# Optimization experiments

Hardware: AMD Instinct MI355X
Metric: run time of the kernel (lower is better)

## Reference

```python
import jax, jax.numpy as jnp
import numpy as np

B, S, D, H = 2, 2048, 1024, 16
DH = D // H
ROPE_BASE = 10000.0


def apply_rope(x):
    # x: [B, H, S, DH]; rotate-half RoPE, base 10000
    half = DH // 2
    inv_freq = 1.0 / (ROPE_BASE ** (jnp.arange(half, dtype=jnp.float32) / half))
    ang = jnp.arange(S, dtype=jnp.float32)[:, None] * inv_freq[None, :]  # [S, half]
    cos = jnp.cos(ang)[None, None]  # [1,1,S,half]
    sin = jnp.sin(ang)[None, None]
    x1, x2 = x[..., :half], x[..., half:]
    return jnp.concatenate([x1 * cos - x2 * sin, x1 * sin + x2 * cos], axis=-1)


def setup_inputs() -> dict:
    key = jax.random.key(0)
    ks = jax.random.split(key, 9)
    w = lambda k: jax.random.normal(k, (D, D), dtype=jnp.float32) * 0.02
    return {
        "x": jax.random.normal(ks[0], (B, S, D), dtype=jnp.float32),
        "Wq": w(ks[1]), "bq": jnp.zeros((D,), jnp.float32),
        "Wk": w(ks[2]), "bk": jnp.zeros((D,), jnp.float32),
        "Wv": w(ks[3]), "bv": jnp.zeros((D,), jnp.float32),
        "Wo": w(ks[4]), "bo": jnp.zeros((D,), jnp.float32),
    }


def reference(x, Wq, bq, Wk, bk, Wv, bv, Wo, bo):
    # projections (W stored as [in, out])
    q = x @ Wq + bq
    k = x @ Wk + bk
    v = x @ Wv + bv
    # [B, S, D] -> [B, H, S, DH]
    to_heads = lambda t: t.reshape(B, S, H, DH).transpose(0, 2, 1, 3)
    q, k, v = to_heads(q), to_heads(k), to_heads(v)
    q = apply_rope(q)
    k = apply_rope(k)
    scores = jnp.einsum("bhqd,bhkd->bhqk", q, k) / jnp.sqrt(jnp.float32(DH))
    causal = jnp.tril(jnp.ones((S, S), dtype=bool))  # [S, S]
    scores = jnp.where(causal[None, None], scores, -jnp.inf)
    probs = jax.nn.softmax(scores, axis=-1)
    ctx = jnp.einsum("bhqk,bhkd->bhqd", probs, v)
    ctx = ctx.transpose(0, 2, 1, 3).reshape(B, S, D)  # concat heads
    return ctx @ Wo + bo
```

## Files before the change

### kernel.cpp

```cpp
#include <hip/hip_runtime.h>
#include <hip/hip_bf16.h>

#define B_  2
#define S_  2048
#define D_  1024
#define H_  16
#define DH_ 64

typedef __attribute__((ext_vector_type(8))) short bf16x8;
typedef __attribute__((ext_vector_type(4))) float f32x4;

__device__ __forceinline__ short f2bf(float f) {
  unsigned int u; __builtin_memcpy(&u, &f, 4);
  u = (u + 0x7FFFu + ((u >> 16) & 1u)) >> 16;
  return (short)u;
}
__device__ __forceinline__ unsigned cvtpk(float a, float b) {
  unsigned r;
  asm("v_cvt_pk_bf16_f32 %0, %1, %2" : "=v"(r) : "v"(a), "v"(b));
  return r;
}

#define GLOAD_LDS16(gp, lp) \
  __builtin_amdgcn_global_load_lds((const __attribute__((address_space(1))) void*)(gp), \
                                   (__attribute__((address_space(3))) void*)(lp), 16, 0, 0)

#define MFMA16(a, b, c) __builtin_amdgcn_mfma_f32_16x16x32_bf16(a, b, c, 0, 0, 0)

#define RAW_BARRIER() do {                                   \
    asm volatile("s_waitcnt lgkmcnt(0)" ::: "memory");       \
    __builtin_amdgcn_s_barrier();                            \
    asm volatile("" ::: "memory");                           \
  } while (0)

union U8 { unsigned u[4]; bf16x8 v; };

__global__ __launch_bounds__(256) void k_cvt_table(const float* __restrict__ in,
                                                   short* __restrict__ out,
                                                   float* __restrict__ cosT,
                                                   float* __restrict__ sinT) {
  int bid = blockIdx.x;
  if (bid < 4096) {
    int i = bid * 256 + threadIdx.x;
    float4 v = ((const float4*)in)[i];
    short4 o; o.x = f2bf(v.x); o.y = f2bf(v.y); o.z = f2bf(v.z); o.w = f2bf(v.w);
    *(short4*)(out + (size_t)i * 4) = o;
  } else {
    int i = (bid - 4096) * 256 + threadIdx.x;
    int s = i >> 5, d = i & 31;
    float invf = exp2f(-(float)d * (13.287712379549449f / 32.0f));
    float ang = (float)s * invf;
    cosT[i] = cosf(ang);
    sinT[i] = sinf(ang);
  }
}

__global__ __launch_bounds__(256) void k_transpose4(const float* __restrict__ W0,
                                                    const float* __restrict__ W1,
                                                    const float* __restrict__ W2,
                                                    const float* __restrict__ W3,
                                                    short* __restrict__ WtBase) {
  __shared__ float tile[32][33];
  const float* W = (blockIdx.z == 0) ? W0 : (blockIdx.z == 1) ? W1 :
                   (blockIdx.z == 2) ? W2 : W3;
  short* Wt = WtBase + (size_t)blockIdx.z * D_ * D_;
  int tx = threadIdx.x, ty = threadIdx.y;
  int bx = blockIdx.x * 32, by = blockIdx.y * 32;
  #pragma unroll
  for (int i = 0; i < 32; i += 8)
    tile[ty + i][tx] = W[(size_t)(by + ty + i) * D_ + bx + tx];
  __syncthreads();
  #pragma unroll
  for (int i = 0; i < 32; i += 8)
    Wt[(size_t)(bx + ty + i) * D_ + by + tx] = f2bf(tile[tx][ty + i]);
}

__global__ __launch_bounds__(256) void k_gemm_qkv(const short* __restrict__ A,
                                                  const short* __restrict__ Bt,
                                                  const float* __restrict__ bq,
                                                  const float* __restrict__ bk,
                                                  const float* __restrict__ bv,
                                                  const float* __restrict__ cosT,
                                                  const float* __restrict__ sinT,
                                                  short* __restrict__ qb,
                                                  short* __restrict__ kb,
                                                  short* __restrict__ vb) {
  const int K = 1024;
  __shared__ __align__(16) short lA[128 * 32];
  __shared__ __align__(16) short lB[128 * 32];
  const int fid = blockIdx.y * 24 + blockIdx.x;
  const int swz = (fid & 7) * 96 + (fid >> 3);
  const int bxs = swz % 24, bys = swz / 24;
  const int tid = threadIdx.x;
  const int wid = tid >> 6, lane = tid & 63;
  const int brow = bys * 128, bcol = bxs * 128;
  const int wr = wid >> 1, wc = wid & 1;
  const int g = lane >> 4, c15 = lane & 15;
  const int sr = lane >> 2, scol = (lane & 3) * 8;
  f32x4 acc[4][4] = {};

  for (int kt = 0; kt < K; kt += 32) {
    __syncthreads();
    #pragma unroll
    for (int ch = 0; ch < 2; ++ch) {
      const short* ga = A + (size_t)(brow + ch * 64 + wid * 16 + sr) * K + kt + scol;
      const short* gb = Bt + (size_t)(bcol + ch * 64 + wid * 16 + sr) * K + kt + scol;
      GLOAD_LDS16(ga, &lA[(ch * 64 + wid * 16) * 32]);
      GLOAD_LDS16(gb, &lB[(ch * 64 + wid * 16) * 32]);
    }
    __syncthreads();
    bf16x8 af[4], bfr[4];
    #pragma unroll
    for (int mi = 0; mi < 4; ++mi)
      af[mi] = *(const bf16x8*)&lA[(wr * 64 + mi * 16 + c15) * 32 + g * 8];
    #pragma unroll
    for (int ni = 0; ni < 4; ++ni)
      bfr[ni] = *(const bf16x8*)&lB[(wc * 64 + ni * 16 + c15) * 32 + g * 8];
    #pragma unroll
    for (int mi = 0; mi < 4; ++mi)
      #pragma unroll
      for (int ni = 0; ni < 4; ++ni)
        acc[mi][ni] = MFMA16(af[mi], bfr[ni], acc[mi][ni]);
  }

  const int seg = bcol >> 10;
  const float* bp = (seg == 0) ? bq : (seg == 1) ? bk : bv;
  short* dst = (seg == 0) ? qb : (seg == 1) ? kb : vb;
  const float alpha = (seg == 0) ? 0.18033688f : 1.0f;
  const bool rope = (seg < 2);
  #pragma unroll
  for (int mi = 0; mi < 4; ++mi) {
    #pragma unroll
    for (int ni = 0; ni < 2; ++ni) {
      int col  = bcol + wc * 64 + ni * 16 + c15;
      int lcol = col & 1023;
      int d    = col & 63;
      float b1 = bp[lcol], b2 = bp[lcol + 32];
      #pragma unroll
      for (int r = 0; r < 4; ++r) {
        int row = brow + wr * 64 + mi * 16 + g * 4 + r;
        float x1 = (acc[mi][ni][r]     + b1) * alpha;
        float x2 = (acc[mi][ni + 2][r] + b2) * alpha;
        float o1 = x1, o2 = x2;
        if (rope) {
          int s = row & (S_ - 1);
          float co = cosT[s * 32 + d], si = sinT[s * 32 + d];
          o1 = x1 * co - x2 * si;
          o2 = x1 * si + x2 * co;
        }
        dst[(size_t)row * 1024 + lcol]      = f2bf(o1);
        dst[(size_t)row * 1024 + lcol + 32] = f2bf(o2);
      }
    }
  }
}

__global__ __launch_bounds__(256) void k_gemm(const short* __restrict__ A,
                                              const short* __restrict__ Bt,
                                              const float* __restrict__ bias,
                                              float* __restrict__ out,
                                              int M, int N, int K) {
  __shared__ __align__(16) short lA[128 * 32];
  __shared__ __align__(16) short lB[128 * 32];
  const int fid = blockIdx.y * 8 + blockIdx.x;
  const int swz = (fid & 7) * 32 + (fid >> 3);
  const int bxs = swz % 8, bys = swz / 8;
  const int tid = threadIdx.x;
  const int wid = tid >> 6, lane = tid & 63;
  const int brow = bys * 128, bcol = bxs * 128;
  const int wr = wid >> 1, wc = wid & 1;
  const int g = lane >> 4, c15 = lane & 15;
  const int sr = lane >> 2, scol = (lane & 3) * 8;
  f32x4 acc[4][4] = {};

  for (int kt = 0; kt < K; kt += 32) {
    __syncthreads();
    #pragma unroll
    for (int ch = 0; ch < 2; ++ch) {
      const short* ga = A + (size_t)(brow + ch * 64 + wid * 16 + sr) * K + kt + scol;
      const short* gb = Bt + (size_t)(bcol + ch * 64 + wid * 16 + sr) * K + kt + scol;
      GLOAD_LDS16(ga, &lA[(ch * 64 + wid * 16) * 32]);
      GLOAD_LDS16(gb, &lB[(ch * 64 + wid * 16) * 32]);
    }
    __syncthreads();
    bf16x8 af[4], bfr[4];
    #pragma unroll
    for (int mi = 0; mi < 4; ++mi)
      af[mi] = *(const bf16x8*)&lA[(wr * 64 + mi * 16 + c15) * 32 + g * 8];
    #pragma unroll
    for (int ni = 0; ni < 4; ++ni)
      bfr[ni] = *(const bf16x8*)&lB[(wc * 64 + ni * 16 + c15) * 32 + g * 8];
    #pragma unroll
    for (int mi = 0; mi < 4; ++mi)
      #pragma unroll
      for (int ni = 0; ni < 4; ++ni)
        acc[mi][ni] = MFMA16(af[mi], bfr[ni], acc[mi][ni]);
  }

  #pragma unroll
  for (int mi = 0; mi < 4; ++mi) {
    #pragma unroll
    for (int ni = 0; ni < 4; ++ni) {
      int col = bcol + wc * 64 + ni * 16 + c15;
      float bv = bias[col];
      #pragma unroll
      for (int r = 0; r < 4; ++r) {
        int row = brow + wr * 64 + mi * 16 + g * 4 + r;
        out[(size_t)row * N + col] = acc[mi][ni][r] + bv;
      }
    }
  }
}

__device__ __forceinline__ void softmax_g(f32x4 (&s)[4], float& m, float& l,
                                          f32x4 (&o)[4], int g) {
  float pm = -1e30f;
  #pragma unroll
  for (int n = 0; n < 4; ++n)
    #pragma unroll
    for (int r = 0; r < 4; ++r) pm = fmaxf(pm, s[n][r]);
  pm = fmaxf(pm, __shfl_xor(pm, 16));
  pm = fmaxf(pm, __shfl_xor(pm, 32));
  if (!__all(pm <= m + 8.0f)) {
    float nm = fmaxf(m, pm);
    float corr = exp2f(m - nm);
    m = nm; l *= corr;
    float cf[4];
    #pragma unroll
    for (int r = 0; r < 4; ++r) cf[r] = __shfl(corr, g * 4 + r);
    #pragma unroll
    for (int dblk = 0; dblk < 4; ++dblk)
      #pragma unroll
      for (int r = 0; r < 4; ++r) o[dblk][r] *= cf[r];
  }
  float rs = 0.0f;
  #pragma unroll
  for (int n = 0; n < 4; ++n)
    #pragma unroll
    for (int r = 0; r < 4; ++r) {
      float p = exp2f(s[n][r] - m);
      s[n][r] = p; rs += p;
    }
  rs += __shfl_xor(rs, 16);
  rs += __shfl_xor(rs, 32);
  l += rs;
}

__device__ __forceinline__ void build_pa(const f32x4 (&s)[4], U8 (&pa)[2],
                                         int g, int c15) {
  unsigned pk[4][2];
  #pragma unroll
  for (int n = 0; n < 4; ++n) {
    pk[n][0] = cvtpk(s[n][0], s[n][1]);
    pk[n][1] = cvtpk(s[n][2], s[n][3]);
  }
  #pragma unroll
  for (int kh = 0; kh < 2; ++kh) {
    #pragma unroll
    for (int widx = 0; widx < 4; ++widx) {
      int src = (2 * (g & 1) + (widx >> 1)) * 16 + c15;
      unsigned lo = __shfl(pk[2 * kh][widx & 1], src);
      unsigned hi = __shfl(pk[2 * kh + 1][widx & 1], src);
      pa[kh].u[widx] = (g & 2) ? hi : lo;
    }
  }
}

__global__ __launch_bounds__(256, 4) void k_flash(const short* __restrict__ Qb,
                                                  const short* __restrict__ Kb,
                                                  const short* __restrict__ Vb,
                                                  short* __restrict__ Ctx,
                                                  float* __restrict__ pO,
                                                  float* __restrict__ pML) {
  __shared__ __align__(16) short Vt[2][64][72];
  __shared__ __align__(16) short Kl[2][4096];
  const int bid = blockIdx.x;
  const int sched = bid >> 5, bh = bid & 31;
  int qt, t0, t1, sid = 0; bool split;
  if (sched < 19) { qt = 18 - sched; t0 = 0; t1 = qt; split = false; }
  else {
    int j = sched - 19; qt = 31 - (j >> 1);
    int h1 = (qt + 2) >> 1;
    if ((j & 1) == 0) { t0 = h1; t1 = qt; }
    else              { t0 = 0;  t1 = h1 - 1; }
    split = true; sid = bh * 26 + j;
  }
  const int b   = bh >> 4, h = bh & 15;
  const int tid = threadIdx.x, w = tid >> 6, lane = tid & 63;
  const int g   = lane >> 4, c15 = lane & 15;
  const int qg0 = qt * 64 + w * 16;
  const int qabs = qg0 + c15;

  const short* qp = Qb + ((size_t)(b * S_ + qabs)) * D_ + h * DH_ + g * 8;
  bf16x8 qf0 = *(const bf16x8*)qp;
  bf16x8 qf1 = *(const bf16x8*)(qp + 32);

  const int vkv = lane;
  const int vd0 = w * 16;
  const int vcol = vkv ^ (w << 3);
  const short* vrow = Vb + (size_t)b * S_ * D_ + h * DH_ + vd0;

  const short* kbase = Kb + (size_t)b * S_ * D_ + h * DH_;
  const int kidx0 = w * 128 + lane;
  const int kkv0 = kidx0 >> 3, kdb0 = (kidx0 & 7) ^ (kkv0 & 7);
  const int kidx1 = kidx0 + 64;
  const int kkv1 = kidx1 >> 3, kdb1 = (kidx1 & 7) ^ (kkv1 & 7);

  f32x4 o[4] = {};
  float m = -1e30f, l = 0.0f;

  bf16x8 kc0, kc1, vc0, vc1, kn0, kn1, vn0, vn1;

  {
    const short* kb0 = kbase + (size_t)(t0 * 64) * D_;
    bf16x8 tk0 = *(const bf16x8*)(kb0 + (size_t)kkv0 * D_ + kdb0 * 8);
    bf16x8 tk1 = *(const bf16x8*)(kb0 + (size_t)kkv1 * D_ + kdb1 * 8);
    const short* vp = vrow + (size_t)(t0 * 64 + vkv) * D_;
    bf16x8 tv0 = *(const bf16x8*)vp;
    bf16x8 tv1 = *(const bf16x8*)(vp + 8);
    *(bf16x8*)&Kl[t0 & 1][kidx0 * 8] = tk0;
    *(bf16x8*)&Kl[t0 & 1][kidx1 * 8] = tk1;
    #pragma unroll
    for (int j = 0; j < 8; ++j) Vt[t0 & 1][vd0 + j][vcol] = tv0[j];
    #pragma unroll
    for (int j = 0; j < 8; ++j) Vt[t0 & 1][vd0 + 8 + j][vcol] = tv1[j];
    if (t0 + 1 <= t1) {
      const short* kb1 = kbase + (size_t)((t0 + 1) * 64) * D_;
      kc0 = *(const bf16x8*)(kb1 + (size_t)kkv0 * D_ + kdb0 * 8);
      kc1 = *(const bf16x8*)(kb1 + (size_t)kkv1 * D_ + kdb1 * 8);
      const short* vp1 = vrow + (size_t)((t0 + 1) * 64 + vkv) * D_;
      vc0 = *(const bf16x8*)vp1;
      vc1 = *(const bf16x8*)(vp1 + 8);
    }
  }
  RAW_BARRIER();

#define FBODY(T, KC0, KC1, VC0, VC1, KN0, KN1, VN0, VN1) do {                   \
    const int kv0 = (T) * 64;                                                   \
    if ((T) + 2 <= t1) {                                                        \
      const short* kb2 = kbase + (size_t)(kv0 + 128) * D_;                      \
      KN0 = *(const bf16x8*)(kb2 + (size_t)kkv0 * D_ + kdb0 * 8);               \
      KN1 = *(const bf16x8*)(kb2 + (size_t)kkv1 * D_ + kdb1 * 8);               \
      const short* vp2 = vrow + (size_t)(kv0 + 128 + vkv) * D_;                 \
      VN0 = *(const bf16x8*)vp2;                                                \
      VN1 = *(const bf16x8*)(vp2 + 8);                                          \
    }                                                                           \
    if (kv0 <= qg0 + 15) {                                                      \
      const short* ks = &Kl[(T) & 1][0];                                        \
      f32x4 s[4] = {};                                                          \
      __builtin_amdgcn_s_setprio(1);                                            \
      _Pragma("unroll")                                                         \
      for (int n = 0; n < 4; ++n) {                                             \
        int krow = (n * 16 + c15) * 64;                                         \
        bf16x8 k0 = *(const bf16x8*)&ks[krow + ((g ^ (c15 & 7)) * 8)];          \
        bf16x8 k1 = *(const bf16x8*)&ks[krow + (((g + 4) ^ (c15 & 7)) * 8)];    \
        s[n] = MFMA16(k0, qf0, s[n]);                                           \
        s[n] = MFMA16(k1, qf1, s[n]);                                           \
      }                                                                         \
      __builtin_amdgcn_s_setprio(0);                                            \
      if (kv0 + 63 > qg0) {                                                     \
        _Pragma("unroll")                                                       \
        for (int n = 0; n < 4; ++n)                                             \
          _Pragma("unroll")                                                     \
          for (int r = 0; r < 4; ++r)                                           \
            if (kv0 + n * 16 + g * 4 + r > qabs) s[n][r] = -1e30f;              \
      }                                                                         \
      softmax_g(s, m, l, o, g);                                                 \
      U8 pa[2];                                                                 \
      build_pa(s, pa, g, c15);                                                  \
      __builtin_amdgcn_s_setprio(1);                                            \
      _Pragma("unroll")                                                         \
      for (int kh = 0; kh < 2; ++kh)                                            \
        _Pragma("unroll")                                                       \
        for (int dblk = 0; dblk < 4; ++dblk) {                                  \
          bf16x8 vbf = *(const bf16x8*)&Vt[(T) & 1][dblk * 16 + c15]            \
                                         [kh * 32 + ((g ^ dblk) * 8)];          \
          o[dblk] = MFMA16(pa[kh].v, vbf, o[dblk]);                             \
        }                                                                       \
      __builtin_amdgcn_s_setprio(0);                                            \
    }                                                                           \
    if ((T) + 1 <= t1) {                                                        \
      *(bf16x8*)&Kl[((T) + 1) & 1][kidx0 * 8] = KC0;                            \
      *(bf16x8*)&Kl[((T) + 1) & 1][kidx1 * 8] = KC1;                            \
      _Pragma("unroll")                                                         \
      for (int j = 0; j < 8; ++j) Vt[((T) + 1) & 1][vd0 + j][vcol] = VC0[j];    \
      _Pragma("unroll")                                                         \
      for (int j = 0; j < 8; ++j) Vt[((T) + 1) & 1][vd0 + 8 + j][vcol] = VC1[j];\
      RAW_BARRIER();                                                            \
    }                                                                           \
  } while (0)

  for (int t = t0; t <= t1; ) {
    FBODY(t, kc0, kc1, vc0, vc1, kn0, kn1, vn0, vn1);
    ++t;
    if (t > t1) break;
    FBODY(t, kn0, kn1, vn0, vn1, kc0, kc1, vc0, vc1);
    ++t;
  }
#undef FBODY

  if (!split) {
    float linv = 1.0f / l;
    float lf[4];
    #pragma unroll
    for (int r = 0; r < 4; ++r) lf[r] = __shfl(linv, g * 4 + r);
    #pragma unroll
    for (int dblk = 0; dblk < 4; ++dblk)
      #pragma unroll
      for (int r = 0; r < 4; ++r) {
        int q = qg0 + g * 4 + r;
        Ctx[((size_t)(b * S_ + q)) * D_ + h * DH_ + dblk * 16 + c15] = f2bf(o[dblk][r] * lf[r]);
      }
  } else {
    float* po = pO + ((size_t)sid * 64 + w * 16) * 64;
    #pragma unroll
    for (int dblk = 0; dblk < 4; ++dblk)
      #pragma unroll
      for (int r = 0; r < 4; ++r)
        po[(g * 4 + r) * 64 + dblk * 16 + c15] = o[dblk][r];
    if (lane < 16) {
      pML[(size_t)sid * 128 + w * 16 + lane]      = m;
      pML[(size_t)sid * 128 + 64 + w * 16 + lane] = l;
    }
  }
}

__global__ __launch_bounds__(256) void k_combine(const float* __restrict__ pO,
                                                 const float* __restrict__ pML,
                                                 short* __restrict__ Ctx) {
  const int p = blockIdx.x;
  const int qt = 19 + (p >> 5), bh = p & 31;
  const int b = bh >> 4, h = bh & 15;
  const int jb = (31 - qt) * 2;
  const int sidB = bh * 26 + jb;
  const int sidA = bh * 26 + jb + 1;
  const int q = threadIdx.x >> 2;
  const int d0 = (threadIdx.x & 3) * 16;
  float mA = pML[(size_t)sidA * 128 + q], lA = pML[(size_t)sidA * 128 + 64 + q];
  float mB = pML[(size_t)sidB * 128 + q], lB = pML[(size_t)sidB * 128 + 64 + q];
  float M = fmaxf(mA, mB);
  float wA = exp2f(mA - M), wB = exp2f(mB - M);
  float inv = 1.0f / (lA * wA + lB * wB);
  const float* oA = pO + ((size_t)sidA * 64 + q) * 64 + d0;
  const float* oB = pO + ((size_t)sidB * 64 + q) * 64 + d0;
  short* cp = Ctx + ((size_t)(b * S_ + qt * 64 + q)) * D_ + h * DH_ + d0;
  #pragma unroll
  for (int i = 0; i < 16; i += 4) {
    float4 a = *(const float4*)(oA + i);
    float4 c = *(const float4*)(oB + i);
    cp[i + 0] = f2bf((a.x * wA + c.x * wB) * inv);
    cp[i + 1] = f2bf((a.y * wA + c.y * wB) * inv);
    cp[i + 2] = f2bf((a.z * wA + c.z * wB) * inv);
    cp[i + 3] = f2bf((a.w * wA + c.w * wB) * inv);
  }
}

extern "C" void kernel_launch(void* const* d_in, const int* in_sizes, int n_in,
                              void* d_out, int out_size, void* d_ws, size_t ws_size,
                              hipStream_t stream) {
  (void)in_sizes; (void)n_in; (void)out_size; (void)ws_size;
  const float* x  = (const float*)d_in[0];
  const float* Wq = (const float*)d_in[1];
  const float* bq = (const float*)d_in[2];
  const float* Wk = (const float*)d_in[3];
  const float* bk = (const float*)d_in[4];
  const float* Wv = (const float*)d_in[5];
  const float* bv = (const float*)d_in[6];
  const float* Wo = (const float*)d_in[7];
  const float* bo = (const float*)d_in[8];
  float* out = (float*)d_out;
  char* ws = (char*)d_ws;

  const size_t MS = (size_t)B_ * S_;
  short* xb  = (short*)(ws);
  short* wqT = (short*)(ws + (size_t)8 * 1024 * 1024);
  short* wkT = wqT + (size_t)D_ * D_;
  short* wvT = wkT + (size_t)D_ * D_;
  short* woT = wvT + (size_t)D_ * D_;
  short* qb  = (short*)(ws + (size_t)16 * 1024 * 1024);
  short* kb  = qb + MS * D_;
  short* vb  = kb + MS * D_;
  short* ctx = vb + MS * D_;
  float* cosT = (float*)(ws + (size_t)48 * 1024 * 1024);
  float* sinT = cosT + (size_t)S_ * 32;
  float* pO  = (float*)(ws);
  float* pML = (float*)(ws + (size_t)48 * 1024 * 1024 + 512 * 1024);

  k_cvt_table<<<dim3(4096 + 256), 256, 0, stream>>>(x, xb, cosT, sinT);
  k_transpose4<<<dim3(32, 32, 4), dim3(32, 8), 0, stream>>>(Wq, Wk, Wv, Wo, wqT);
  k_gemm_qkv<<<dim3(24, 32), 256, 0, stream>>>(xb, wqT, bq, bk, bv, cosT, sinT, qb, kb, vb);
  k_flash<<<dim3(45 * 32), 256, 0, stream>>>(qb, kb, vb, ctx, pO, pML);
  k_combine<<<dim3(13 * 32), 256, 0, stream>>>(pO, pML, ctx);
  k_gemm<<<dim3(8, 32), 256, 0, stream>>>(ctx, woT, bo, out, 4096, 1024, 1024);
}
```

Measured before the change: 135.6 us.

## Load K fragments directly from global memory instead of staging through LDS

Drops the double-buffered K shared-memory tile and its register prefetch. Each wave now reads its K MFMA operands straight from global memory (relying on L1/L2 to share them across the four waves), and the launch bound rises to 8 blocks per CU. The aim is to cut LDS footprint and register pressure so occupancy increases. The cost is that K loads are no longer prefetched, so their latency sits on the critical path before the QK MFMAs, each wave issues its own redundant global loads, and the per-wave causal skip of fully masked tiles is gone.

```diff
diff --git a/kernel.cpp b/kernel.cpp
--- a/kernel.cpp
+++ b/kernel.cpp
@@ -266,14 +266,13 @@
   }
 }
 
-__global__ __launch_bounds__(256, 4) void k_flash(const short* __restrict__ Qb,
+__global__ __launch_bounds__(256, 8) void k_flash(const short* __restrict__ Qb,
                                                   const short* __restrict__ Kb,
                                                   const short* __restrict__ Vb,
                                                   short* __restrict__ Ctx,
                                                   float* __restrict__ pO,
                                                   float* __restrict__ pML) {
   __shared__ __align__(16) short Vt[2][64][72];
-  __shared__ __align__(16) short Kl[2][4096];
   const int bid = blockIdx.x;
   const int sched = bid >> 5, bh = bid & 31;
   int qt, t0, t1, sid = 0; bool split;
@@ -295,39 +294,27 @@
   bf16x8 qf0 = *(const bf16x8*)qp;
   bf16x8 qf1 = *(const bf16x8*)(qp + 32);
 
+  const short* kbase = Kb + (size_t)b * S_ * D_ + h * DH_ + g * 8;
+
   const int vkv = lane;
   const int vd0 = w * 16;
   const int vcol = vkv ^ (w << 3);
   const short* vrow = Vb + (size_t)b * S_ * D_ + h * DH_ + vd0;
 
-  const short* kbase = Kb + (size_t)b * S_ * D_ + h * DH_;
-  const int kidx0 = w * 128 + lane;
-  const int kkv0 = kidx0 >> 3, kdb0 = (kidx0 & 7) ^ (kkv0 & 7);
-  const int kidx1 = kidx0 + 64;
-  const int kkv1 = kidx1 >> 3, kdb1 = (kidx1 & 7) ^ (kkv1 & 7);
-
   f32x4 o[4] = {};
   float m = -1e30f, l = 0.0f;
 
-  bf16x8 kc0, kc1, vc0, vc1, kn0, kn1, vn0, vn1;
+  bf16x8 vc0, vc1, vn0, vn1;
 
   {
-    const short* kb0 = kbase + (size_t)(t0 * 64) * D_;
-    bf16x8 tk0 = *(const bf16x8*)(kb0 + (size_t)kkv0 * D_ + kdb0 * 8);
-    bf16x8 tk1 = *(const bf16x8*)(kb0 + (size_t)kkv1 * D_ + kdb1 * 8);
     const short* vp = vrow + (size_t)(t0 * 64 + vkv) * D_;
     bf16x8 tv0 = *(const bf16x8*)vp;
     bf16x8 tv1 = *(const bf16x8*)(vp + 8);
-    *(bf16x8*)&Kl[t0 & 1][kidx0 * 8] = tk0;
-    *(bf16x8*)&Kl[t0 & 1][kidx1 * 8] = tk1;
     #pragma unroll
     for (int j = 0; j < 8; ++j) Vt[t0 & 1][vd0 + j][vcol] = tv0[j];
     #pragma unroll
     for (int j = 0; j < 8; ++j) Vt[t0 & 1][vd0 + 8 + j][vcol] = tv1[j];
     if (t0 + 1 <= t1) {
-      const short* kb1 = kbase + (size_t)((t0 + 1) * 64) * D_;
-      kc0 = *(const bf16x8*)(kb1 + (size_t)kkv0 * D_ + kdb0 * 8);
-      kc1 = *(const bf16x8*)(kb1 + (size_t)kkv1 * D_ + kdb1 * 8);
       const short* vp1 = vrow + (size_t)((t0 + 1) * 64 + vkv) * D_;
       vc0 = *(const bf16x8*)vp1;
       vc1 = *(const bf16x8*)(vp1 + 8);
@@ -335,25 +322,21 @@
   }
   RAW_BARRIER();
 
-#define FBODY(T, KC0, KC1, VC0, VC1, KN0, KN1, VN0, VN1) do {                   \
+#define FBODY(T, VC0, VC1, VN0, VN1) do {                                       \
     const int kv0 = (T) * 64;                                                   \
     if ((T) + 2 <= t1) {                                                        \
-      const short* kb2 = kbase + (size_t)(kv0 + 128) * D_;                      \
-      KN0 = *(const bf16x8*)(kb2 + (size_t)kkv0 * D_ + kdb0 * 8);               \
-      KN1 = *(const bf16x8*)(kb2 + (size_t)kkv1 * D_ + kdb1 * 8);               \
       const short* vp2 = vrow + (size_t)(kv0 + 128 + vkv) * D_;                 \
       VN0 = *(const bf16x8*)vp2;                                                \
       VN1 = *(const bf16x8*)(vp2 + 8);                                          \
     }                                                                           \
-    if (kv0 <= qg0 + 15) {                                                      \
-      const short* ks = &Kl[(T) & 1][0];                                        \
+    {                                                                           \
+      const short* kp = kbase + (size_t)(kv0 + c15) * D_;                       \
       f32x4 s[4] = {};                                                          \
       __builtin_amdgcn_s_setprio(1);                                            \
       _Pragma("unroll")                                                         \
       for (int n = 0; n < 4; ++n) {                                             \
-        int krow = (n * 16 + c15) * 64;                                         \
-        bf16x8 k0 = *(const bf16x8*)&ks[krow + ((g ^ (c15 & 7)) * 8)];          \
-        bf16x8 k1 = *(const bf16x8*)&ks[krow + (((g + 4) ^ (c15 & 7)) * 8)];    \
+        bf16x8 k0 = *(const bf16x8*)(kp + (size_t)n * 16 * D_);                 \
+        bf16x8 k1 = *(const bf16x8*)(kp + (size_t)n * 16 * D_ + 32);            \
         s[n] = MFMA16(k0, qf0, s[n]);                                           \
         s[n] = MFMA16(k1, qf1, s[n]);                                           \
       }                                                                         \
@@ -380,8 +363,6 @@
       __builtin_amdgcn_s_setprio(0);                                            \
     }                                                                           \
     if ((T) + 1 <= t1) {                                                        \
-      *(bf16x8*)&Kl[((T) + 1) & 1][kidx0 * 8] = KC0;                            \
-      *(bf16x8*)&Kl[((T) + 1) & 1][kidx1 * 8] = KC1;                            \
       _Pragma("unroll")                                                         \
       for (int j = 0; j < 8; ++j) Vt[((T) + 1) & 1][vd0 + j][vcol] = VC0[j];    \
       _Pragma("unroll")                                                         \
@@ -391,10 +372,10 @@
   } while (0)
 
   for (int t = t0; t <= t1; ) {
-    FBODY(t, kc0, kc1, vc0, vc1, kn0, kn1, vn0, vn1);
+    FBODY(t, vc0, vc1, vn0, vn1);
     ++t;
     if (t > t1) break;
-    FBODY(t, kn0, kn1, vn0, vn1, kc0, kc1, vc0, vc1);
+    FBODY(t, vn0, vn1, vc0, vc1);
     ++t;
   }
 #undef FBODY
```

Result: slower. 216.4 us (+59.6%).

## Double-buffer GEMM LDS tiles and merge prep kernels into one launch

Applied to the files above, without the earlier changes.

Both GEMM kernels now use two LDS buffers per operand. The next K-tile is issued via global_load_lds while the current tile is consumed by MFMAs, with a vmcnt wait and a single barrier per step in place of two syncthreads around a blocking load. Separately, the fp32-to-bf16 conversion/RoPE-table kernel and the weight transpose kernel are fused into one launch to drop a kernel boundary. The GEMMs now use double the LDS, which may reduce occupancy, and the pipeline correctness depends on the vmcnt counting being right.

```diff
diff --git a/kernel.cpp b/kernel.cpp
--- a/kernel.cpp
+++ b/kernel.cpp
@@ -35,44 +35,45 @@
 
 union U8 { unsigned u[4]; bf16x8 v; };
 
-__global__ __launch_bounds__(256) void k_cvt_table(const float* __restrict__ in,
-                                                   short* __restrict__ out,
-                                                   float* __restrict__ cosT,
-                                                   float* __restrict__ sinT) {
-  int bid = blockIdx.x;
+__global__ __launch_bounds__(256) void k_prep(const float* __restrict__ in,
+                                              short* __restrict__ out,
+                                              float* __restrict__ cosT,
+                                              float* __restrict__ sinT,
+                                              const float* __restrict__ W0,
+                                              const float* __restrict__ W1,
+                                              const float* __restrict__ W2,
+                                              const float* __restrict__ W3,
+                                              short* __restrict__ WtBase) {
+  __shared__ float tile[32][33];
+  const int bid = blockIdx.x;
+  const int tid = threadIdx.x;
   if (bid < 4096) {
-    int i = bid * 256 + threadIdx.x;
+    int i = bid * 256 + tid;
     float4 v = ((const float4*)in)[i];
     short4 o; o.x = f2bf(v.x); o.y = f2bf(v.y); o.z = f2bf(v.z); o.w = f2bf(v.w);
     *(short4*)(out + (size_t)i * 4) = o;
-  } else {
-    int i = (bid - 4096) * 256 + threadIdx.x;
+  } else if (bid < 4352) {
+    int i = (bid - 4096) * 256 + tid;
     int s = i >> 5, d = i & 31;
     float invf = exp2f(-(float)d * (13.287712379549449f / 32.0f));
     float ang = (float)s * invf;
     cosT[i] = cosf(ang);
     sinT[i] = sinf(ang);
-  }
-}
-
-__global__ __launch_bounds__(256) void k_transpose4(const float* __restrict__ W0,
-                                                    const float* __restrict__ W1,
-                                                    const float* __restrict__ W2,
-                                                    const float* __restrict__ W3,
-                                                    short* __restrict__ WtBase) {
-  __shared__ float tile[32][33];
-  const float* W = (blockIdx.z == 0) ? W0 : (blockIdx.z == 1) ? W1 :
-                   (blockIdx.z == 2) ? W2 : W3;
-  short* Wt = WtBase + (size_t)blockIdx.z * D_ * D_;
-  int tx = threadIdx.x, ty = threadIdx.y;
-  int bx = blockIdx.x * 32, by = blockIdx.y * 32;
-  #pragma unroll
-  for (int i = 0; i < 32; i += 8)
-    tile[ty + i][tx] = W[(size_t)(by + ty + i) * D_ + bx + tx];
-  __syncthreads();
-  #pragma unroll
-  for (int i = 0; i < 32; i += 8)
-    Wt[(size_t)(bx + ty + i) * D_ + by + tx] = f2bf(tile[tx][ty + i]);
+  } else {
+    const int p = bid - 4352;
+    const int z = p >> 10, rem = p & 1023;
+    const float* W = (z == 0) ? W0 : (z == 1) ? W1 : (z == 2) ? W2 : W3;
+    short* Wt = WtBase + (size_t)z * D_ * D_;
+    const int tx = tid & 31, ty = tid >> 5;
+    const int bx = (rem & 31) * 32, by = (rem >> 5) * 32;
+    #pragma unroll
+    for (int i = 0; i < 32; i += 8)
+      tile[ty + i][tx] = W[(size_t)(by + ty + i) * D_ + bx + tx];
+    __syncthreads();
+    #pragma unroll
+    for (int i = 0; i < 32; i += 8)
+      Wt[(size_t)(bx + ty + i) * D_ + by + tx] = f2bf(tile[tx][ty + i]);
+  }
 }
 
 __global__ __launch_bounds__(256) void k_gemm_qkv(const short* __restrict__ A,
@@ -85,9 +86,9 @@
                                                   short* __restrict__ qb,
                                                   short* __restrict__ kb,
                                                   short* __restrict__ vb) {
-  const int K = 1024;
-  __shared__ __align__(16) short lA[128 * 32];
-  __shared__ __align__(16) short lB[128 * 32];
+  const int K = 1024, NT = 32;
+  __shared__ __align__(16) short lA[2][128 * 32];
+  __shared__ __align__(16) short lB[2][128 * 32];
   const int fid = blockIdx.y * 24 + blockIdx.x;
   const int swz = (fid & 7) * 96 + (fid >> 3);
   const int bxs = swz % 24, bys = swz / 24;
@@ -99,28 +100,43 @@
   const int sr = lane >> 2, scol = (lane & 3) * 8;
   f32x4 acc[4][4] = {};
 
-  for (int kt = 0; kt < K; kt += 32) {
-    __syncthreads();
-    #pragma unroll
-    for (int ch = 0; ch < 2; ++ch) {
-      const short* ga = A + (size_t)(brow + ch * 64 + wid * 16 + sr) * K + kt + scol;
-      const short* gb = Bt + (size_t)(bcol + ch * 64 + wid * 16 + sr) * K + kt + scol;
-      GLOAD_LDS16(ga, &lA[(ch * 64 + wid * 16) * 32]);
-      GLOAD_LDS16(gb, &lB[(ch * 64 + wid * 16) * 32]);
-    }
-    __syncthreads();
+  const short* arow = A  + (size_t)(brow + wid * 16 + sr) * K + scol;
+  const short* brow_ = Bt + (size_t)(bcol + wid * 16 + sr) * K + scol;
+
+  #pragma unroll
+  for (int ch = 0; ch < 2; ++ch) {
+    GLOAD_LDS16(arow + (size_t)(ch * 64) * K, &lA[0][(ch * 64 + wid * 16) * 32]);
+    GLOAD_LDS16(brow_ + (size_t)(ch * 64) * K, &lB[0][(ch * 64 + wid * 16) * 32]);
+  }
+
+  for (int it = 0; it < NT; ++it) {
+    const int cur = it & 1;
+    if (it + 1 < NT) {
+      const int kt2 = (it + 1) * 32;
+      #pragma unroll
+      for (int ch = 0; ch < 2; ++ch) {
+        GLOAD_LDS16(arow + (size_t)(ch * 64) * K + kt2, &lA[cur ^ 1][(ch * 64 + wid * 16) * 32]);
+        GLOAD_LDS16(brow_ + (size_t)(ch * 64) * K + kt2, &lB[cur ^ 1][(ch * 64 + wid * 16) * 32]);
+      }
+      asm volatile("s_waitcnt vmcnt(4)" ::: "memory");
+    } else {
+      asm volatile("s_waitcnt vmcnt(0)" ::: "memory");
+    }
+    __builtin_amdgcn_s_barrier();
+    asm volatile("" ::: "memory");
     bf16x8 af[4], bfr[4];
     #pragma unroll
     for (int mi = 0; mi < 4; ++mi)
-      af[mi] = *(const bf16x8*)&lA[(wr * 64 + mi * 16 + c15) * 32 + g * 8];
+      af[mi] = *(const bf16x8*)&lA[cur][(wr * 64 + mi * 16 + c15) * 32 + g * 8];
     #pragma unroll
     for (int ni = 0; ni < 4; ++ni)
-      bfr[ni] = *(const bf16x8*)&lB[(wc * 64 + ni * 16 + c15) * 32 + g * 8];
+      bfr[ni] = *(const bf16x8*)&lB[cur][(wc * 64 + ni * 16 + c15) * 32 + g * 8];
     #pragma unroll
     for (int mi = 0; mi < 4; ++mi)
       #pragma unroll
       for (int ni = 0; ni < 4; ++ni)
         acc[mi][ni] = MFMA16(af[mi], bfr[ni], acc[mi][ni]);
+    RAW_BARRIER();
   }
 
   const int seg = bcol >> 10;
@@ -160,8 +176,9 @@
                                               const float* __restrict__ bias,
                                               float* __restrict__ out,
                                               int M, int N, int K) {
-  __shared__ __align__(16) short lA[128 * 32];
-  __shared__ __align__(16) short lB[128 * 32];
+  const int NT = 32;
+  __shared__ __align__(16) short lA[2][128 * 32];
+  __shared__ __align__(16) short lB[2][128 * 32];
   const int fid = blockIdx.y * 8 + blockIdx.x;
   const int swz = (fid & 7) * 32 + (fid >> 3);
   const int bxs = swz % 8, bys = swz / 8;
@@ -173,28 +190,43 @@
   const int sr = lane >> 2, scol = (lane & 3) * 8;
   f32x4 acc[4][4] = {};
 
-  for (int kt = 0; kt < K; kt += 32) {
-    __syncthreads();
-    #pragma unroll
-    for (int ch = 0; ch < 2; ++ch) {
-      const short* ga = A + (size_t)(brow + ch * 64 + wid * 16 + sr) * K + kt + scol;
-      const short* gb = Bt + (size_t)(bcol + ch * 64 + wid * 16 + sr) * K + kt + scol;
-      GLOAD_LDS16(ga, &lA[(ch * 64 + wid * 16) * 32]);
-      GLOAD_LDS16(gb, &lB[(ch * 64 + wid * 16) * 32]);
-    }
-    __syncthreads();
+  const short* arow = A  + (size_t)(brow + wid * 16 + sr) * K + scol;
+  const short* brow_ = Bt + (size_t)(bcol + wid * 16 + sr) * K + scol;
+
+  #pragma unroll
+  for (int ch = 0; ch < 2; ++ch) {
+    GLOAD_LDS16(arow + (size_t)(ch * 64) * K, &lA[0][(ch * 64 + wid * 16) * 32]);
+    GLOAD_LDS16(brow_ + (size_t)(ch * 64) * K, &lB[0][(ch * 64 + wid * 16) * 32]);
+  }
+
+  for (int it = 0; it < NT; ++it) {
+    const int cur = it & 1;
+    if (it + 1 < NT) {
+      const int kt2 = (it + 1) * 32;
+      #pragma unroll
+      for (int ch = 0; ch < 2; ++ch) {
+        GLOAD_LDS16(arow + (size_t)(ch * 64) * K + kt2, &lA[cur ^ 1][(ch * 64 + wid * 16) * 32]);
+        GLOAD_LDS16(brow_ + (size_t)(ch * 64) * K + kt2, &lB[cur ^ 1][(ch * 64 + wid * 16) * 32]);
+      }
+      asm volatile("s_waitcnt vmcnt(4)" ::: "memory");
+    } else {
+      asm volatile("s_waitcnt vmcnt(0)" ::: "memory");
+    }
+    __builtin_amdgcn_s_barrier();
+    asm volatile("" ::: "memory");
     bf16x8 af[4], bfr[4];
     #pragma unroll
     for (int mi = 0; mi < 4; ++mi)
-      af[mi] = *(const bf16x8*)&lA[(wr * 64 + mi * 16 + c15) * 32 + g * 8];
+      af[mi] = *(const bf16x8*)&lA[cur][(wr * 64 + mi * 16 + c15) * 32 + g * 8];
     #pragma unroll
     for (int ni = 0; ni < 4; ++ni)
-      bfr[ni] = *(const bf16x8*)&lB[(wc * 64 + ni * 16 + c15) * 32 + g * 8];
+      bfr[ni] = *(const bf16x8*)&lB[cur][(wc * 64 + ni * 16 + c15) * 32 + g * 8];
     #pragma unroll
     for (int mi = 0; mi < 4; ++mi)
       #pragma unroll
       for (int ni = 0; ni < 4; ++ni)
         acc[mi][ni] = MFMA16(af[mi], bfr[ni], acc[mi][ni]);
+    RAW_BARRIER();
   }
 
   #pragma unroll
@@ -486,8 +518,7 @@
   float* pO  = (float*)(ws);
   float* pML = (float*)(ws + (size_t)48 * 1024 * 1024 + 512 * 1024);
 
-  k_cvt_table<<<dim3(4096 + 256), 256, 0, stream>>>(x, xb, cosT, sinT);
-  k_transpose4<<<dim3(32, 32, 4), dim3(32, 8), 0, stream>>>(Wq, Wk, Wv, Wo, wqT);
+  k_prep<<<dim3(8448), 256, 0, stream>>>(x, xb, cosT, sinT, Wq, Wk, Wv, Wo, wqT);
   k_gemm_qkv<<<dim3(24, 32), 256, 0, stream>>>(xb, wqT, bq, bk, bv, cosT, sinT, qb, kb, vb);
   k_flash<<<dim3(45 * 32), 256, 0, stream>>>(qb, kb, vb, ctx, pO, pML);
   k_combine<<<dim3(13 * 32), 256, 0, stream>>>(pO, pML, ctx);
```

Result: slower. 139.9 us (+3.2%).

## Software-pipeline QK^T of next tile with softmax and PV of previous tile

Applied to the files above, without the earlier changes.

Restructures the flash-attention inner loop so each iteration computes the QK^T scores for tile T while running softmax and the PV MFMA for tile T-1, using two alternating score register buffers. The V tile load and store to LDS are shifted one stage later to match, and an epilogue handles the last tile's softmax and PV. The goal is to overlap softmax ALU work with MFMA work and hide latency. In exchange it adds register pressure, drops the per-wave early skip of fully masked tiles, and places a barrier on every iteration.

```diff
diff --git a/kernel.cpp b/kernel.cpp
--- a/kernel.cpp
+++ b/kernel.cpp
@@ -308,6 +308,8 @@
 
   f32x4 o[4] = {};
   float m = -1e30f, l = 0.0f;
+  f32x4 sA[4], sB[4];
+  bool havep = false;
 
   bf16x8 kc0, kc1, vc0, vc1, kn0, kn1, vn0, vn1;
 
@@ -315,47 +317,42 @@
     const short* kb0 = kbase + (size_t)(t0 * 64) * D_;
     bf16x8 tk0 = *(const bf16x8*)(kb0 + (size_t)kkv0 * D_ + kdb0 * 8);
     bf16x8 tk1 = *(const bf16x8*)(kb0 + (size_t)kkv1 * D_ + kdb1 * 8);
-    const short* vp = vrow + (size_t)(t0 * 64 + vkv) * D_;
-    bf16x8 tv0 = *(const bf16x8*)vp;
-    bf16x8 tv1 = *(const bf16x8*)(vp + 8);
     *(bf16x8*)&Kl[t0 & 1][kidx0 * 8] = tk0;
     *(bf16x8*)&Kl[t0 & 1][kidx1 * 8] = tk1;
-    #pragma unroll
-    for (int j = 0; j < 8; ++j) Vt[t0 & 1][vd0 + j][vcol] = tv0[j];
-    #pragma unroll
-    for (int j = 0; j < 8; ++j) Vt[t0 & 1][vd0 + 8 + j][vcol] = tv1[j];
+    const short* vp = vrow + (size_t)(t0 * 64 + vkv) * D_;
+    vc0 = *(const bf16x8*)vp;
+    vc1 = *(const bf16x8*)(vp + 8);
     if (t0 + 1 <= t1) {
       const short* kb1 = kbase + (size_t)((t0 + 1) * 64) * D_;
       kc0 = *(const bf16x8*)(kb1 + (size_t)kkv0 * D_ + kdb0 * 8);
       kc1 = *(const bf16x8*)(kb1 + (size_t)kkv1 * D_ + kdb1 * 8);
-      const short* vp1 = vrow + (size_t)((t0 + 1) * 64 + vkv) * D_;
-      vc0 = *(const bf16x8*)vp1;
-      vc1 = *(const bf16x8*)(vp1 + 8);
     }
   }
   RAW_BARRIER();
 
-#define FBODY(T, KC0, KC1, VC0, VC1, KN0, KN1, VN0, VN1) do {                   \
+#define FBODY(T, KC0, KC1, VC0, VC1, KN0, KN1, VN0, VN1, SC, SP) do {           \
     const int kv0 = (T) * 64;                                                   \
     if ((T) + 2 <= t1) {                                                        \
       const short* kb2 = kbase + (size_t)(kv0 + 128) * D_;                      \
       KN0 = *(const bf16x8*)(kb2 + (size_t)kkv0 * D_ + kdb0 * 8);               \
       KN1 = *(const bf16x8*)(kb2 + (size_t)kkv1 * D_ + kdb1 * 8);               \
-      const short* vp2 = vrow + (size_t)(kv0 + 128 + vkv) * D_;                 \
+    }                                                                           \
+    if ((T) + 1 <= t1) {                                                        \
+      const short* vp2 = vrow + (size_t)(kv0 + 64 + vkv) * D_;                  \
       VN0 = *(const bf16x8*)vp2;                                                \
       VN1 = *(const bf16x8*)(vp2 + 8);                                          \
     }                                                                           \
-    if (kv0 <= qg0 + 15) {                                                      \
+    {                                                                           \
       const short* ks = &Kl[(T) & 1][0];                                        \
-      f32x4 s[4] = {};                                                          \
       __builtin_amdgcn_s_setprio(1);                                            \
       _Pragma("unroll")                                                         \
       for (int n = 0; n < 4; ++n) {                                             \
         int krow = (n * 16 + c15) * 64;                                         \
         bf16x8 k0 = *(const bf16x8*)&ks[krow + ((g ^ (c15 & 7)) * 8)];          \
         bf16x8 k1 = *(const bf16x8*)&ks[krow + (((g + 4) ^ (c15 & 7)) * 8)];    \
-        s[n] = MFMA16(k0, qf0, s[n]);                                           \
-        s[n] = MFMA16(k1, qf1, s[n]);                                           \
+        f32x4 z = {0.0f, 0.0f, 0.0f, 0.0f};                                     \
+        z = MFMA16(k0, qf0, z);                                                 \
+        SC[n] = MFMA16(k1, qf1, z);                                             \
       }                                                                         \
       __builtin_amdgcn_s_setprio(0);                                            \
       if (kv0 + 63 > qg0) {                                                     \
@@ -363,41 +360,65 @@
         for (int n = 0; n < 4; ++n)                                             \
           _Pragma("unroll")                                                     \
           for (int r = 0; r < 4; ++r)                                           \
-            if (kv0 + n * 16 + g * 4 + r > qabs) s[n][r] = -1e30f;              \
+            if (kv0 + n * 16 + g * 4 + r > qabs) SC[n][r] = -1e30f;             \
       }                                                                         \
-      softmax_g(s, m, l, o, g);                                                 \
+    }                                                                           \
+    if (havep) {                                                                \
+      softmax_g(SP, m, l, o, g);                                                \
       U8 pa[2];                                                                 \
-      build_pa(s, pa, g, c15);                                                  \
+      build_pa(SP, pa, g, c15);                                                 \
       __builtin_amdgcn_s_setprio(1);                                            \
       _Pragma("unroll")                                                         \
       for (int kh = 0; kh < 2; ++kh)                                            \
         _Pragma("unroll")                                                       \
         for (int dblk = 0; dblk < 4; ++dblk) {                                  \
-          bf16x8 vbf = *(const bf16x8*)&Vt[(T) & 1][dblk * 16 + c15]            \
+          bf16x8 vbf = *(const bf16x8*)&Vt[((T) + 1) & 1][dblk * 16 + c15]      \
                                          [kh * 32 + ((g ^ dblk) * 8)];          \
           o[dblk] = MFMA16(pa[kh].v, vbf, o[dblk]);                             \
         }                                                                       \
       __builtin_amdgcn_s_setprio(0);                                            \
     }                                                                           \
+    havep = true;                                                               \
     if ((T) + 1 <= t1) {                                                        \
       *(bf16x8*)&Kl[((T) + 1) & 1][kidx0 * 8] = KC0;                            \
       *(bf16x8*)&Kl[((T) + 1) & 1][kidx1 * 8] = KC1;                            \
-      _Pragma("unroll")                                                         \
-      for (int j = 0; j < 8; ++j) Vt[((T) + 1) & 1][vd0 + j][vcol] = VC0[j];    \
-      _Pragma("unroll")                                                         \
-      for (int j = 0; j < 8; ++j) Vt[((T) + 1) & 1][vd0 + 8 + j][vcol] = VC1[j];\
-      RAW_BARRIER();                                                            \
     }                                                                           \
+    _Pragma("unroll")                                                           \
+    for (int j = 0; j < 8; ++j) Vt[(T) & 1][vd0 + j][vcol] = VC0[j];            \
+    _Pragma("unroll")                                                           \
+    for (int j = 0; j < 8; ++j) Vt[(T) & 1][vd0 + 8 + j][vcol] = VC1[j];        \
+    RAW_BARRIER();                                                              \
   } while (0)
 
   for (int t = t0; t <= t1; ) {
-    FBODY(t, kc0, kc1, vc0, vc1, kn0, kn1, vn0, vn1);
+    FBODY(t, kc0, kc1, vc0, vc1, kn0, kn1, vn0, vn1, sA, sB);
     ++t;
     if (t > t1) break;
-    FBODY(t, kn0, kn1, vn0, vn1, kc0, kc1, vc0, vc1);
+    FBODY(t, kn0, kn1, vn0, vn1, kc0, kc1, vc0, vc1, sB, sA);
     ++t;
   }
 #undef FBODY
+
+  if (havep) {
+    U8 pa[2];
+    if (((t1 - t0) & 1) == 0) {
+      softmax_g(sA, m, l, o, g);
+      build_pa(sA, pa, g, c15);
+    } else {
+      softmax_g(sB, m, l, o, g);
+      build_pa(sB, pa, g, c15);
+    }
+    __builtin_amdgcn_s_setprio(1);
+    #pragma unroll
+    for (int kh = 0; kh < 2; ++kh)
+      #pragma unroll
+      for (int dblk = 0; dblk < 4; ++dblk) {
+        bf16x8 vbf = *(const bf16x8*)&Vt[t1 & 1][dblk * 16 + c15]
+                                       [kh * 32 + ((g ^ dblk) * 8)];
+        o[dblk] = MFMA16(pa[kh].v, vbf, o[dblk]);
+      }
+    __builtin_amdgcn_s_setprio(0);
+  }
 
   if (!split) {
     float linv = 1.0f / l;
```

New measurement: 293.1 us. +116.1%, slower.
